# Optimization experiments

Measured on AMD Instinct MI355X. Metric: run time of the kernel, lower is better.

Reference implementation:

```python
import jax, jax.numpy as jnp
import numpy as np

B, T, D, H, DK, DV, FF = 4, 1024, 1024, 16, 64, 64, 4096


def setup_inputs() -> dict:
    key = jax.random.key(0)
    ks = jax.random.split(key, 16)
    sc = 0.02  # init scale (original uses uninitialized torch.empty; use small randn)
    n = lambda k, shape: jax.random.normal(k, shape, jnp.float32) * sc
    return dict(
        x=jax.random.normal(ks[0], (B, T, D), jnp.float32),
        y=jax.random.normal(ks[1], (B, T, D), jnp.float32),
        Wq1=n(ks[2], (H, D, DK)), Wk1=n(ks[3], (H, D, DK)),
        Wv1=n(ks[4], (H, D, DV)), Wo1=n(ks[5], (D, D)),
        Wq2=n(ks[6], (H, D, DK)), Wk2=n(ks[7], (H, D, DK)),
        Wv2=n(ks[8], (H, D, DV)), Wo2=n(ks[9], (D, D)),
        W_in=n(ks[10], (FF, D)), b_in=jnp.zeros((FF,), jnp.float32),
        W_out=n(ks[11], (D, FF)), b_out=jnp.zeros((D,), jnp.float32),
    )


def _mha(q, k, v, Wq, Wk, Wv, Wo):
    # per-head projections: (B,T,D) x (H,D,dk) -> (B,H,T,dk)
    WQ = jnp.einsum('btd,hdk->bhtk', q, Wq)
    WK = jnp.einsum('bsd,hdk->bhsk', k, Wk)
    WV = jnp.einsum('bsd,hdv->bhsv', v, Wv)
    scores = jnp.einsum('bhtk,bhsk->bhts', WQ, WK) / jnp.sqrt(jnp.float32(DK))
    # NOTE: original code softmaxes over dim=2 (the QUERY axis), kept faithfully
    attn = jax.nn.softmax(scores, axis=2)
    partial = jnp.einsum('bhts,bhsv->bhtv', attn, WV)
    partial = partial.transpose(0, 2, 1, 3).reshape(q.shape[0], q.shape[1], -1)  # (B,T,H*dv)
    return partial @ Wo


def _sub_norm(o):
    mean = o.mean(-1, keepdims=True)
    std = o.std(-1, ddof=1, keepdims=True)  # torch.std default is unbiased
    return o - mean - std  # faithful: subtract (not divide by) std


def reference(x, y, Wq1, Wk1, Wv1, Wo1, Wq2, Wk2, Wv2, Wo2, W_in, b_in, W_out, b_out):
    out1 = _sub_norm(_mha(y, y, y, Wq1, Wk1, Wv1, Wo1) + y)
    out2 = _sub_norm(_mha(y, x, x, Wq2, Wk2, Wv2, Wo2) + out1)
    ff = jax.nn.relu(y @ W_in.T + b_in) @ W_out.T + b_out  # FFN applied to y, as in source
    return _sub_norm(ff + out2)
```

## Files before the change

kernel.cpp:

```cpp
#include <hip/hip_runtime.h>


typedef unsigned short u16;
typedef __bf16 bf16x8 __attribute__((ext_vector_type(8)));
typedef float f32x4 __attribute__((ext_vector_type(4)));

__device__ __forceinline__ u16 f2bf(float f) {
    unsigned int u = __float_as_uint(f);
    u += 0x7fffu + ((u >> 16) & 1u);
    return (u16)(u >> 16);
}
__device__ __forceinline__ float bf2f(u16 b) {
    return __uint_as_float(((unsigned int)b) << 16);
}

typedef __attribute__((address_space(1))) const void* as1cv;
typedef __attribute__((address_space(3))) void* as3v;
__device__ __forceinline__ void gl_lds16(const void* g, void* l) {
    __builtin_amdgcn_global_load_lds((as1cv)g, (as3v)l, 16, 0, 0);
}


__global__ __launch_bounds__(256) void convert_f2b_k(const float* __restrict__ in, u16* __restrict__ out) {
    long i = (long)blockIdx.x * 256 + threadIdx.x;
    float4 v = reinterpret_cast<const float4*>(in)[i];
    ushort4 o;
    o.x = f2bf(v.x); o.y = f2bf(v.y); o.z = f2bf(v.z); o.w = f2bf(v.w);
    reinterpret_cast<ushort4*>(out)[i] = o;
}

__global__ __launch_bounds__(256) void pack_perm_t(const float* __restrict__ in, u16* __restrict__ out,
                                                   int Q, int R) {
    __shared__ float tile[64][65];
    int p = blockIdx.z;
    int r0 = blockIdx.x * 64, q0 = blockIdx.y * 64;
    int tx = threadIdx.x & 63, ty = threadIdx.x >> 6;
    const float* inp = in + ((long)p * Q + q0) * R + r0;
    #pragma unroll
    for (int i = 0; i < 64; i += 4)
        tile[ty + i][tx] = inp[(long)(ty + i) * R + tx];
    __syncthreads();
    u16* outp = out + ((long)p * R + r0) * Q + q0;
    #pragma unroll
    for (int i = 0; i < 64; i += 4)
        outp[(long)(ty + i) * Q + tx] = f2bf(tile[tx][ty + i]);
}

__global__ __launch_bounds__(256) void transpose_k(const u16* __restrict__ in, long ld_in, long z_in,
                                                   u16* __restrict__ out, long ld_out, long z_out) {
    __shared__ u16 tile[64][66];
    const u16* inz = in + (long)blockIdx.z * z_in;
    u16* outz = out + (long)blockIdx.z * z_out;
    int r0 = blockIdx.y * 64;
    int c0 = blockIdx.x * 64;
    int tx = threadIdx.x & 63, ty = threadIdx.x >> 6;
    #pragma unroll
    for (int i = 0; i < 64; i += 4)
        tile[ty + i][tx] = inz[(long)(r0 + ty + i) * ld_in + c0 + tx];
    __syncthreads();
    #pragma unroll
    for (int i = 0; i < 64; i += 4)
        outz[(long)(c0 + ty + i) * ld_out + r0 + tx] = tile[tx][ty + i];
}

template<int BM, int BN, int BK, int WM, int WN, int OUT_BF16, int EPI, int SWZ, int KS>
__global__ __launch_bounds__(256) void gemm_k(
    const u16* __restrict__ A, long lda, long a_zin, long a_zout,
    const u16* __restrict__ B, long ldb, long b_zin, long b_zout,
    void* __restrict__ Cv, long ldc, long c_zin, long c_zout,
    int zin, int K, float alpha, const float* __restrict__ bias,
    float* __restrict__ csum)
{
    static_assert(BK == 64, "staging assumes BK=64");
    constexpr int WTM = BM / WM;
    constexpr int WTN = BN / WN;
    constexpr int TM = WTM / 16;
    constexpr int TN = WTN / 16;
    __shared__ __align__(16) u16 smem[(BM + BN) * BK];
    u16* As = smem;
    u16* Bs = smem + BM * BK;

    int bx, by, z;
    if (SWZ == 4) {
        int L = blockIdx.x;
        if (KS > 1) { z = L >> 9; L &= 511; } else { z = 0; }
        by = (L & 7) * 4 + ((L >> 3) & 3);
        bx = L >> 5;
    } else {
        bx = blockIdx.x; by = blockIdx.y; z = blockIdx.z;
    }
    int zi = z % zin, zo = z / zin;
    A += (long)zi * a_zin + (long)zo * a_zout;
    B += (long)zi * b_zin + (long)zo * b_zout;
    long coff = (long)zi * c_zin + (long)zo * c_zout;

    int tid = threadIdx.x;
    int lane = tid & 63;
    int wave = tid >> 6;
    int wm = wave / WN, wn = wave % WN;
    long bm0 = (long)by * BM, bn0 = (long)bx * BN;

    f32x4 acc[TM][TN];
    #pragma unroll
    for (int i = 0; i < TM; ++i)
        #pragma unroll
        for (int j = 0; j < TN; ++j) {
            acc[i][j][0] = 0.f; acc[i][j][1] = 0.f;
            acc[i][j][2] = 0.f; acc[i][j][3] = 0.f;
        }

    int r16 = lane & 15;
    int quad = lane >> 4;
    int l8 = lane >> 3;
    int gsw = ((lane & 7) ^ l8) * 8;

    constexpr int ASTR = BM / 8;
    constexpr int BSTR = BN / 8;

    for (int k0 = 0; k0 < K; k0 += BK) {
        #pragma unroll
        for (int s = wave; s < ASTR; s += 4)
            gl_lds16(&A[(bm0 + s * 8 + l8) * lda + k0 + gsw], &As[s * 512]);
        #pragma unroll
        for (int s = wave; s < BSTR; s += 4)
            gl_lds16(&B[(bn0 + s * 8 + l8) * ldb + k0 + gsw], &Bs[s * 512]);
        __syncthreads();
        #pragma unroll
        for (int kk = 0; kk < BK; kk += 32) {
            int cb = (kk >> 3) + quad;
            bf16x8 av[TM], bv[TN];
            #pragma unroll
            for (int i = 0; i < TM; ++i) {
                int r = wm * WTM + i * 16 + r16;
                av[i] = *reinterpret_cast<const bf16x8*>(&As[r * 64 + ((cb ^ (r & 7)) * 8)]);
            }
            #pragma unroll
            for (int j = 0; j < TN; ++j) {
                int r = wn * WTN + j * 16 + r16;
                bv[j] = *reinterpret_cast<const bf16x8*>(&Bs[r * 64 + ((cb ^ (r & 7)) * 8)]);
            }
            #pragma unroll
            for (int i = 0; i < TM; ++i)
                #pragma unroll
                for (int j = 0; j < TN; ++j)
                    acc[i][j] = __builtin_amdgcn_mfma_f32_16x16x32_bf16(av[i], bv[j], acc[i][j], 0, 0, 0);
        }
        __syncthreads();
    }

    int rb = quad * 4;

    if (EPI == 4) {
        float csl[TN];
        #pragma unroll
        for (int j = 0; j < TN; ++j) csl[j] = 0.f;
        #pragma unroll
        for (int i = 0; i < TM; ++i)
            #pragma unroll
            for (int j = 0; j < TN; ++j)
                #pragma unroll
                for (int r = 0; r < 4; ++r)
                    csl[j] += __expf(acc[i][j][r] * alpha);
        #pragma unroll
        for (int j = 0; j < TN; ++j) {
            float cs = csl[j];
            cs += __shfl_xor(cs, 16, 64);
            cs += __shfl_xor(cs, 32, 64);
            if (quad == 0) {
                long col = bn0 + wn * WTN + j * 16 + r16;
                atomicAdd(&csum[((long)zo * zin + zi) * 1024 + col], cs);
            }
        }
        return;
    }

    constexpr int EB = OUT_BF16 ? 2 : 4;
    constexpr int CH = 16 / EB;
    constexpr int STRIDE = BN + CH;
    constexpr int LDSB = (BM + BN) * BK * 2;
    constexpr int EPASS = (BM * STRIDE * EB > LDSB) ? 2 : 1;
    constexpr int RPP = BM / EPASS;
    static_assert(RPP * STRIDE * EB <= LDSB, "epilogue tile overflows LDS");
    static_assert(EPASS == 1 || (WM == 2 && WTM == RPP), "pass/wave row alignment");
    constexpr int CPR = BN / CH;
    constexpr int NCH = RPP * CPR / 256;
    static_assert(RPP * CPR % 256 == 0, "store mapping");

    float* Ef = reinterpret_cast<float*>(smem);
    char* Cb = reinterpret_cast<char*>(Cv);

    for (int pass = 0; pass < EPASS; ++pass) {
        int p0 = pass * RPP;
        __syncthreads();
        #pragma unroll
        for (int i = 0; i < TM; ++i) {
            #pragma unroll
            for (int j = 0; j < TN; ++j) {
                int lcol = wn * WTN + j * 16 + r16;
                float bsv = (EPI == 1 || EPI == 2) ? bias[bn0 + lcol] : 0.f;
                #pragma unroll
                for (int r = 0; r < 4; ++r) {
                    int lrow = wm * WTM + i * 16 + rb + r;
                    if ((unsigned)(lrow - p0) < (unsigned)RPP) {
                        float v = acc[i][j][r] * alpha;
                        if (EPI == 1) { v += bsv; v = v > 0.f ? v : 0.f; }
                        else if (EPI == 2) { v += bsv; }
                        if (OUT_BF16) smem[(lrow - p0) * STRIDE + lcol] = f2bf(v);
                        else          Ef[(lrow - p0) * STRIDE + lcol] = v;
                    }
                }
            }
        }
        __syncthreads();
        #pragma unroll
        for (int c = 0; c < NCH; ++c) {
            int cid = tid + c * 256;
            int row = cid / CPR, ch = cid - row * CPR;
            int4 v = *reinterpret_cast<const int4*>(
                reinterpret_cast<const char*>(smem) + (row * STRIDE + ch * CH) * EB);
            long gidx = coff + (bm0 + p0 + row) * ldc + bn0 + ch * CH;
            *reinterpret_cast<int4*>(Cb + gidx * EB) = v;
        }
    }
}

__global__ __launch_bounds__(256) void attn_pv_k(
    const u16* __restrict__ Qg, long ldq, long qbz,
    const u16* __restrict__ Kg, long ldk, long kbz,
    const u16* __restrict__ Vg,
    u16* __restrict__ outg)
{
    __shared__ __align__(16) u16 Qs[128 * 64];
    __shared__ __align__(16) u16 Ks[64 * 64];
    __shared__ __align__(16) u16 Vs[64 * 64];
    __shared__ __align__(16) u16 Es[128 * 64];

    int L = blockIdx.x;
    int h  = (L & 7) * 2 + ((L >> 3) & 1);
    int tb = (L >> 4) & 7;
    int b  = L >> 7;

    const u16* Q  = Qg + (long)b * qbz + h * 64;
    const u16* Kp = Kg + (long)b * kbz + h * 64;
    const u16* Vp = Vg + (long)b * 1048576 + (long)h * 65536;
    u16* outp = outg + (long)b * 1048576 + (long)tb * 131072 + h * 64;

    int tid = threadIdx.x, lane = tid & 63, wave = tid >> 6;
    int wm = wave >> 1, wn = wave & 1;
    int r16 = lane & 15, quad = lane >> 4, l8 = lane >> 3;
    int gsw = ((lane & 7) ^ l8) * 8;
    long t0 = (long)tb * 128;

    #pragma unroll
    for (int s = wave; s < 16; s += 4)
        gl_lds16(&Q[(t0 + s * 8 + l8) * ldq + gsw], &Qs[s * 512]);

    f32x4 acc[4][2];
    #pragma unroll
    for (int i = 0; i < 4; ++i)
        #pragma unroll
        for (int j = 0; j < 2; ++j) {
            acc[i][j][0] = 0.f; acc[i][j][1] = 0.f;
            acc[i][j][2] = 0.f; acc[i][j][3] = 0.f;
        }

    for (int sc = 0; sc < 16; ++sc) {
        #pragma unroll
        for (int s = wave; s < 8; s += 4) {
            gl_lds16(&Kp[(long)(sc * 64 + s * 8 + l8) * ldk + gsw], &Ks[s * 512]);
            gl_lds16(&Vp[(long)(s * 8 + l8) * 1024 + sc * 64 + gsw], &Vs[s * 512]);
        }
        __syncthreads();

        f32x4 e[4][2];
        #pragma unroll
        for (int i = 0; i < 4; ++i)
            #pragma unroll
            for (int j = 0; j < 2; ++j) {
                e[i][j][0] = 0.f; e[i][j][1] = 0.f;
                e[i][j][2] = 0.f; e[i][j][3] = 0.f;
            }
        #pragma unroll
        for (int kk = 0; kk < 64; kk += 32) {
            int cb = (kk >> 3) + quad;
            bf16x8 av[4], bv[2];
            #pragma unroll
            for (int i = 0; i < 4; ++i) {
                int r = wm * 64 + i * 16 + r16;
                av[i] = *reinterpret_cast<const bf16x8*>(&Qs[r * 64 + ((cb ^ (r & 7)) * 8)]);
            }
            #pragma unroll
            for (int j = 0; j < 2; ++j) {
                int r = wn * 32 + j * 16 + r16;
                bv[j] = *reinterpret_cast<const bf16x8*>(&Ks[r * 64 + ((cb ^ (r & 7)) * 8)]);
            }
            #pragma unroll
            for (int i = 0; i < 4; ++i)
                #pragma unroll
                for (int j = 0; j < 2; ++j)
                    e[i][j] = __builtin_amdgcn_mfma_f32_16x16x32_bf16(av[i], bv[j], e[i][j], 0, 0, 0);
        }
        #pragma unroll
        for (int i = 0; i < 4; ++i)
            #pragma unroll
            for (int j = 0; j < 2; ++j) {
                int lcol = wn * 32 + j * 16 + r16;
                #pragma unroll
                for (int r = 0; r < 4; ++r) {
                    int lrow = wm * 64 + i * 16 + quad * 4 + r;
                    float v = __expf(e[i][j][r] * 0.125f);
                    Es[lrow * 64 + (((lcol >> 3) ^ (lrow & 7)) * 8) + (lcol & 7)] = f2bf(v);
                }
            }
        __syncthreads();

        #pragma unroll
        for (int kk = 0; kk < 64; kk += 32) {
            int cb = (kk >> 3) + quad;
            bf16x8 av[4], bv[2];
            #pragma unroll
            for (int i = 0; i < 4; ++i) {
                int r = wm * 64 + i * 16 + r16;
                av[i] = *reinterpret_cast<const bf16x8*>(&Es[r * 64 + ((cb ^ (r & 7)) * 8)]);
            }
            #pragma unroll
            for (int j = 0; j < 2; ++j) {
                int r = wn * 32 + j * 16 + r16;
                bv[j] = *reinterpret_cast<const bf16x8*>(&Vs[r * 64 + ((cb ^ (r & 7)) * 8)]);
            }
            #pragma unroll
            for (int i = 0; i < 4; ++i)
                #pragma unroll
                for (int j = 0; j < 2; ++j)
                    acc[i][j] = __builtin_amdgcn_mfma_f32_16x16x32_bf16(av[i], bv[j], acc[i][j], 0, 0, 0);
        }
        __syncthreads();
    }

    #pragma unroll
    for (int i = 0; i < 4; ++i)
        #pragma unroll
        for (int j = 0; j < 2; ++j) {
            int lcol = wn * 32 + j * 16 + r16;
            #pragma unroll
            for (int r = 0; r < 4; ++r) {
                int lrow = wm * 64 + i * 16 + quad * 4 + r;
                outp[(long)lrow * 1024 + lcol] = f2bf(acc[i][j][r]);
            }
        }
}

__global__ __launch_bounds__(256) void vscale_k(u16* __restrict__ Vt, const float* __restrict__ csum) {
    long idx = (long)blockIdx.x * 256 + threadIdx.x;
    int slab = (int)(idx >> 17);
    int rem = (int)(idx & 131071);
    int hv = rem >> 7;
    int s8 = (rem & 127) * 8;
    const float* cs = csum + slab * 16384 + (hv >> 6) * 1024 + s8;
    u16* pv = Vt + (long)slab * 1048576 + (long)hv * 1024 + s8;
    ushort4 a = *reinterpret_cast<ushort4*>(pv);
    ushort4 b = *reinterpret_cast<ushort4*>(pv + 4);
    a.x = f2bf(bf2f(a.x) / cs[0]); a.y = f2bf(bf2f(a.y) / cs[1]);
    a.z = f2bf(bf2f(a.z) / cs[2]); a.w = f2bf(bf2f(a.w) / cs[3]);
    b.x = f2bf(bf2f(b.x) / cs[4]); b.y = f2bf(bf2f(b.y) / cs[5]);
    b.z = f2bf(bf2f(b.z) / cs[6]); b.w = f2bf(bf2f(b.w) / cs[7]);
    *reinterpret_cast<ushort4*>(pv) = a;
    *reinterpret_cast<ushort4*>(pv + 4) = b;
}

template<int NP, int BIAS>
__global__ __launch_bounds__(256) void addsn_k(const float* __restrict__ parts, long pstride,
                                               const float* __restrict__ resid,
                                               const float* __restrict__ bias,
                                               float* __restrict__ out) {
    __shared__ float sm[8];
    long row = blockIdx.x;
    int tid = threadIdx.x;
    float4 x = reinterpret_cast<const float4*>(resid + row * 1024)[tid];
    #pragma unroll
    for (int p = 0; p < NP; ++p) {
        float4 a = reinterpret_cast<const float4*>(parts + p * pstride + row * 1024)[tid];
        x.x += a.x; x.y += a.y; x.z += a.z; x.w += a.w;
    }
    if (BIAS) {
        float4 bb = reinterpret_cast<const float4*>(bias)[tid];
        x.x += bb.x; x.y += bb.y; x.z += bb.z; x.w += bb.w;
    }
    float s = x.x + x.y + x.z + x.w;
    for (int o = 32; o > 0; o >>= 1) s += __shfl_down(s, o, 64);
    int lane = tid & 63, w = tid >> 6;
    if (lane == 0) sm[w] = s;
    __syncthreads();
    float mean = (sm[0] + sm[1] + sm[2] + sm[3]) * (1.f / 1024.f);
    float d0 = x.x - mean, d1 = x.y - mean, d2 = x.z - mean, d3 = x.w - mean;
    float q = d0 * d0 + d1 * d1 + d2 * d2 + d3 * d3;
    for (int o = 32; o > 0; o >>= 1) q += __shfl_down(q, o, 64);
    if (lane == 0) sm[w + 4] = q;
    __syncthreads();
    float sd = sqrtf((sm[4] + sm[5] + sm[6] + sm[7]) * (1.f / 1023.f));
    float4 ov;
    ov.x = d0 - sd; ov.y = d1 - sd; ov.z = d2 - sd; ov.w = d3 - sd;
    reinterpret_cast<float4*>(out + row * 1024)[tid] = ov;
}


extern "C" void kernel_launch(void* const* d_in, const int* in_sizes, int n_in,
                              void* d_out, int out_size, void* d_ws, size_t ws_size,
                              hipStream_t stream) {
    (void)in_sizes; (void)n_in; (void)out_size; (void)ws_size;
    const float* xf   = (const float*)d_in[0];
    const float* yf   = (const float*)d_in[1];
    const float* Wq1  = (const float*)d_in[2];
    const float* Wk1  = (const float*)d_in[3];
    const float* Wv1  = (const float*)d_in[4];
    const float* Wo1  = (const float*)d_in[5];
    const float* Wq2  = (const float*)d_in[6];
    const float* Wk2  = (const float*)d_in[7];
    const float* Wv2  = (const float*)d_in[8];
    const float* Wo2  = (const float*)d_in[9];
    const float* W_in = (const float*)d_in[10];
    const float* b_in = (const float*)d_in[11];
    const float* W_out= (const float*)d_in[12];
    const float* b_out= (const float*)d_in[13];

    char* p = (char*)d_ws;
    auto alloc = [&](size_t bytes) { char* r = p; p += bytes; return r; };
    u16*   yb    = (u16*)alloc(8388608);
    u16*   xb    = (u16*)alloc(8388608);
    u16*   W1cat = (u16*)alloc(8388608);
    u16*   Wkv2t = (u16*)alloc(4194304);
    u16*   Wo1t  = (u16*)alloc(2097152);
    u16*   Wo2t  = (u16*)alloc(2097152);
    u16*   Winb  = (u16*)alloc(8388608);
    u16*   Woutb = (u16*)alloc(8388608);
    u16*   QKV   = (u16*)alloc(33554432);
    u16*   KV2   = (u16*)alloc(16777216);
    u16*   Vt    = (u16*)alloc(8388608);
    u16*   Pb    = (u16*)alloc(33554432);
    float* csum  = (float*)alloc(262144);
    u16*   part  = (u16*)alloc(8388608);
    float* gout  = (float*)alloc(33554432);
    float* out1  = (float*)alloc(16777216);

    convert_f2b_k<<<4096, 256, 0, stream>>>(yf, yb);
    convert_f2b_k<<<4096, 256, 0, stream>>>(xf, xb);
    pack_perm_t<<<dim3(1, 16, 16), 256, 0, stream>>>(Wq1, W1cat,           1024, 64);
    pack_perm_t<<<dim3(1, 16, 16), 256, 0, stream>>>(Wk1, W1cat + 1048576, 1024, 64);
    pack_perm_t<<<dim3(1, 16, 16), 256, 0, stream>>>(Wv1, W1cat + 2097152, 1024, 64);
    pack_perm_t<<<dim3(1, 16, 16), 256, 0, stream>>>(Wq2, W1cat + 3145728, 1024, 64);
    pack_perm_t<<<dim3(1, 16, 16), 256, 0, stream>>>(Wk2, Wkv2t,           1024, 64);
    pack_perm_t<<<dim3(1, 16, 16), 256, 0, stream>>>(Wv2, Wkv2t + 1048576, 1024, 64);
    pack_perm_t<<<dim3(16, 16, 1), 256, 0, stream>>>(Wo1, Wo1t,            1024, 1024);
    pack_perm_t<<<dim3(16, 16, 1), 256, 0, stream>>>(Wo2, Wo2t,            1024, 1024);
    convert_f2b_k<<<4096, 256, 0, stream>>>(W_in,  Winb);
    convert_f2b_k<<<4096, 256, 0, stream>>>(W_out, Woutb);

    auto run_attention = [&](const u16* Q, long ldq, long qbz,
                             const u16* Kp, long ldk, long kbz,
                             const u16* Vp, long ldv, long vbz) {
        transpose_k<<<dim3(16, 16, 4), 256, 0, stream>>>(Vp, ldv, vbz, Vt, 1024L, 1048576L);
        hipMemsetAsync(csum, 0, 262144, stream);
        gemm_k<128,128,64,2,2,1,4,0,1><<<dim3(8, 8, 64), 256, 0, stream>>>(
            Q, ldq, 64L, qbz, Kp, ldk, 64L, kbz,
            (void*)Pb, 1024L, 0L, 0L, 16, 64, 0.125f, nullptr, csum);
        vscale_k<<<2048, 256, 0, stream>>>(Vt, csum);
        attn_pv_k<<<512, 256, 0, stream>>>(Q, ldq, qbz, Kp, ldk, kbz, Vt, part);
    };

    gemm_k<128,128,64,2,2,1,0,4,1><<<dim3(32 * 32), 256, 0, stream>>>(
        yb, 1024L, 0L, 0L, W1cat, 1024L, 0L, 0L, (void*)QKV, 4096L, 0L, 0L, 1, 1024, 1.0f, nullptr, nullptr);
    gemm_k<128,128,64,2,2,1,0,4,1><<<dim3(16 * 32), 256, 0, stream>>>(
        xb, 1024L, 0L, 0L, Wkv2t, 1024L, 0L, 0L, (void*)KV2, 2048L, 0L, 0L, 1, 1024, 1.0f, nullptr, nullptr);

    run_attention(QKV, 4096L, 4194304L, QKV + 1024, 4096L, 4194304L, QKV + 2048, 4096L, 4194304L);
    gemm_k<128,64,64,2,2,0,0,4,2><<<dim3(2 * 512), 256, 0, stream>>>(
        part, 1024L, 0L, 512L, Wo1t, 1024L, 0L, 512L,
        (void*)gout, 1024L, 0L, 4194304L, 1, 512, 1.0f, nullptr, nullptr);
    addsn_k<2,0><<<4096, 256, 0, stream>>>(gout, 4194304L, yf, nullptr, out1);

    run_attention(QKV + 3072, 4096L, 4194304L, KV2, 2048L, 2097152L, KV2 + 1024, 2048L, 2097152L);
    gemm_k<128,64,64,2,2,0,0,4,2><<<dim3(2 * 512), 256, 0, stream>>>(
        part, 1024L, 0L, 512L, Wo2t, 1024L, 0L, 512L,
        (void*)gout, 1024L, 0L, 4194304L, 1, 512, 1.0f, nullptr, nullptr);
    addsn_k<2,0><<<4096, 256, 0, stream>>>(gout, 4194304L, out1, nullptr, (float*)d_out);

    gemm_k<128,128,64,2,2,1,1,4,1><<<dim3(32 * 32), 256, 0, stream>>>(
        yb, 1024L, 0L, 0L, Winb, 1024L, 0L, 0L, (void*)Pb, 4096L, 0L, 0L, 1, 1024, 1.0f, b_in, nullptr);
    gemm_k<128,64,64,2,2,0,0,4,2><<<dim3(2 * 512), 256, 0, stream>>>(
        Pb, 4096L, 0L, 2048L, Woutb, 4096L, 0L, 2048L,
        (void*)gout, 1024L, 0L, 4194304L, 1, 2048, 1.0f, nullptr, nullptr);
    addsn_k<2,1><<<4096, 256, 0, stream>>>(gout, 4194304L, (const float*)d_out, b_out, (float*)d_out);
}
```

Baseline: 527.8 us.

## Add 256x256 eight-wave pipelined GEMM for projection and FFN matmuls

Introduces a new 512-thread GEMM kernel with 256x256 tiles and double-buffered LDS filled by direct global-to-LDS loads. Loads are staged in halves and interleaved with MFMA quarters under explicit vmcnt waits, barriers and setprio, so memory traffic overlaps compute. It replaces the QKV, KV2 and FFN-in GEMMs, and turns the FFN-out GEMM into a 4-way split-K whose extra partials go into the QKV buffer and are summed by addsn_k. The aim is higher MFMA utilisation and more tile reuse. In exchange there are fewer blocks, larger LDS use, and the QKV buffer is overwritten at the end.

```diff
diff --git a/kernel.cpp b/kernel.cpp
--- a/kernel.cpp
+++ b/kernel.cpp
@@ -224,6 +224,225 @@
     }
 }
 
+
+__device__ __forceinline__ void bar_raw() {
+    asm volatile("" ::: "memory");
+    __builtin_amdgcn_s_barrier();
+    asm volatile("" ::: "memory");
+}
+
+template<int N> __device__ __forceinline__ void vmw() {
+    if constexpr (N == 10) asm volatile("s_waitcnt vmcnt(10)" ::: "memory");
+    else if constexpr (N == 8) asm volatile("s_waitcnt vmcnt(8)" ::: "memory");
+    else if constexpr (N == 4) asm volatile("s_waitcnt vmcnt(4)" ::: "memory");
+    else if constexpr (N == 2) asm volatile("s_waitcnt vmcnt(2)" ::: "memory");
+    else if constexpr (N == 0) asm volatile("s_waitcnt vmcnt(0)" ::: "memory");
+}
+
+__device__ __forceinline__ void stage_half(const u16* __restrict__ base, long ld, int kt,
+                                           u16* __restrict__ lds, int half, int wave) {
+    const u16* src = base + (long)kt * 64;
+    #pragma unroll
+    for (int u = 0; u < 2; ++u) {
+        int s = half * 16 + u * 8 + wave;
+        gl_lds16(src + (long)(s * 8) * ld, lds + s * 512);
+    }
+}
+
+template<int IH>
+__device__ __forceinline__ void read_a8(bf16x8 (&av)[4][2], const u16* __restrict__ As,
+                                        int wm, int r16, int quad) {
+    #pragma unroll
+    for (int ii = 0; ii < 4; ++ii) {
+        int r = IH * 128 + wm * 64 + ii * 16 + r16;
+        #pragma unroll
+        for (int kx = 0; kx < 2; ++kx)
+            av[ii][kx] = *reinterpret_cast<const bf16x8*>(&As[r * 64 + (((kx * 4 + quad) ^ (r & 7)) * 8)]);
+    }
+}
+
+template<int JH>
+__device__ __forceinline__ void read_b8(bf16x8 (&bv)[2][2], const u16* __restrict__ Bs,
+                                        int wn, int r16, int quad) {
+    #pragma unroll
+    for (int j = 0; j < 2; ++j) {
+        int r = JH * 128 + wn * 32 + j * 16 + r16;
+        #pragma unroll
+        for (int kx = 0; kx < 2; ++kx)
+            bv[j][kx] = *reinterpret_cast<const bf16x8*>(&Bs[r * 64 + (((kx * 4 + quad) ^ (r & 7)) * 8)]);
+    }
+}
+
+template<int IH, int JH>
+__device__ __forceinline__ void mfma_q(f32x4 (&acc)[2][4][2][2],
+                                       const bf16x8 (&av)[4][2], const bf16x8 (&bv)[2][2]) {
+    #pragma unroll
+    for (int kx = 0; kx < 2; ++kx)
+        #pragma unroll
+        for (int ii = 0; ii < 4; ++ii)
+            #pragma unroll
+            for (int j = 0; j < 2; ++j)
+                acc[IH][ii][JH][j] = __builtin_amdgcn_mfma_f32_16x16x32_bf16(
+                    av[ii][kx], bv[j][kx], acc[IH][ii][JH][j], 0, 0, 0);
+}
+
+template<int MODE>
+__device__ __forceinline__ void tile_iter(
+    int t, f32x4 (&acc)[2][4][2][2], bf16x8 (&av)[4][2], bf16x8 (&bvh)[2][2][2],
+    u16* __restrict__ smem, const u16* __restrict__ Ab, long lda,
+    const u16* __restrict__ Bb, long ldb, int wave, int wm, int wn, int r16, int quad)
+{
+    u16* As0 = smem + (t & 1) * 32768;
+    u16* Bs0 = As0 + 16384;
+    u16* As1 = smem + ((t + 1) & 1) * 32768;
+    read_a8<0>(av, As0, wm, r16, quad);
+    read_b8<0>(bvh[0], Bs0, wn, r16, quad);
+    if (MODE < 2) stage_half(Ab, lda, t + 1, As1, 1, wave);
+    vmw<MODE == 0 ? 10 : (MODE == 1 ? 10 : 2)>();
+    bar_raw(); __builtin_amdgcn_sched_barrier(0);
+    __builtin_amdgcn_s_setprio(1);
+    mfma_q<0, 0>(acc, av, bvh[0]);
+    __builtin_amdgcn_s_setprio(0);
+    __builtin_amdgcn_sched_barrier(0);
+    bar_raw();
+    read_b8<1>(bvh[1], Bs0, wn, r16, quad);
+    if (MODE == 0) stage_half(Ab, lda, t + 2, As0, 0, wave);
+    vmw<MODE == 0 ? 10 : (MODE == 1 ? 8 : 0)>();
+    bar_raw(); __builtin_amdgcn_sched_barrier(0);
+    __builtin_amdgcn_s_setprio(1);
+    mfma_q<0, 1>(acc, av, bvh[1]);
+    __builtin_amdgcn_s_setprio(0);
+    __builtin_amdgcn_sched_barrier(0);
+    bar_raw();
+    read_a8<1>(av, As0, wm, r16, quad);
+    if (MODE == 0) stage_half(Bb, ldb, t + 2, Bs0, 0, wave);
+    bar_raw(); __builtin_amdgcn_sched_barrier(0);
+    __builtin_amdgcn_s_setprio(1);
+    mfma_q<1, 0>(acc, av, bvh[0]);
+    __builtin_amdgcn_s_setprio(0);
+    __builtin_amdgcn_sched_barrier(0);
+    bar_raw();
+    if (MODE == 0) stage_half(Bb, ldb, t + 2, Bs0, 1, wave);
+    if (MODE < 2) vmw<MODE == 0 ? 10 : 4>();
+    bar_raw(); __builtin_amdgcn_sched_barrier(0);
+    __builtin_amdgcn_s_setprio(1);
+    mfma_q<1, 1>(acc, av, bvh[1]);
+    __builtin_amdgcn_s_setprio(0);
+    __builtin_amdgcn_sched_barrier(0);
+    bar_raw();
+}
+
+template<int NT, int KS, int EPI, int OUT_BF16>
+__global__ __launch_bounds__(512, 2) void gemm8_k(
+    const u16* __restrict__ A, long lda,
+    const u16* __restrict__ B, long ldb,
+    void* __restrict__ Cv, void* __restrict__ Cv2, long ldc,
+    int K, float alpha, const float* __restrict__ bias, long czs)
+{
+    __shared__ __align__(16) u16 smem[65536];
+
+    int L = blockIdx.x;
+    int z = 0;
+    if (KS > 1) { z = L / (16 * NT); L -= z * 16 * NT; }
+    int by = (L & 7) * 2 + ((L >> 3) & 1);
+    int bx = L >> 4;
+    if (KS > 1) { A += (long)z * K; B += (long)z * K; }
+
+    int tid = threadIdx.x;
+    int lane = tid & 63, wave = tid >> 6;
+    int wm = wave >> 2, wn = wave & 3;
+    int r16 = lane & 15, quad = lane >> 4, l8 = lane >> 3;
+    int gsw = ((lane & 7) ^ l8) * 8;
+    long bm0 = (long)by * 256, bn0 = (long)bx * 256;
+    const u16* Ab = A + (bm0 + l8) * lda + gsw;
+    const u16* Bb = B + (bn0 + l8) * ldb + gsw;
+
+    f32x4 acc[2][4][2][2];
+    #pragma unroll
+    for (int a0 = 0; a0 < 2; ++a0)
+        #pragma unroll
+        for (int a1 = 0; a1 < 4; ++a1)
+            #pragma unroll
+            for (int a2 = 0; a2 < 2; ++a2)
+                #pragma unroll
+                for (int a3 = 0; a3 < 2; ++a3) {
+                    acc[a0][a1][a2][a3][0] = 0.f; acc[a0][a1][a2][a3][1] = 0.f;
+                    acc[a0][a1][a2][a3][2] = 0.f; acc[a0][a1][a2][a3][3] = 0.f;
+                }
+    bf16x8 av[4][2];
+    bf16x8 bvh[2][2][2];
+
+    int T = K >> 6;
+
+    stage_half(Ab, lda, 0, smem,         0, wave);
+    stage_half(Bb, ldb, 0, smem + 16384, 0, wave);
+    stage_half(Bb, ldb, 0, smem + 16384, 1, wave);
+    stage_half(Ab, lda, 0, smem,         1, wave);
+    stage_half(Ab, lda, 1, smem + 32768, 0, wave);
+    stage_half(Bb, ldb, 1, smem + 49152, 0, wave);
+    stage_half(Bb, ldb, 1, smem + 49152, 1, wave);
+    vmw<10>();
+    bar_raw();
+
+    for (int t = 0; t < T - 2; ++t)
+        tile_iter<0>(t, acc, av, bvh, smem, Ab, lda, Bb, ldb, wave, wm, wn, r16, quad);
+    tile_iter<1>(T - 2, acc, av, bvh, smem, Ab, lda, Bb, ldb, wave, wm, wn, r16, quad);
+    tile_iter<2>(T - 1, acc, av, bvh, smem, Ab, lda, Bb, ldb, wave, wm, wn, r16, quad);
+
+    constexpr int EB = OUT_BF16 ? 2 : 4;
+    constexpr int EPASS = OUT_BF16 ? 1 : 2;
+    char* Cb = reinterpret_cast<char*>((KS > 1 && z >= 2) ? Cv2 : Cv);
+    if (KS > 1) Cb += (long)(z & 1) * czs * EB;
+    float bsv[2][2];
+    if (EPI == 1) {
+        #pragma unroll
+        for (int jh = 0; jh < 2; ++jh)
+            #pragma unroll
+            for (int j = 0; j < 2; ++j)
+                bsv[jh][j] = bias[bn0 + jh * 128 + wn * 32 + j * 16 + r16];
+    }
+    u16* sm16 = smem;
+    float* smf = reinterpret_cast<float*>(smem);
+    #pragma unroll
+    for (int pass = 0; pass < EPASS; ++pass) {
+        bar_raw();
+        #pragma unroll
+        for (int ih = 0; ih < 2; ++ih) {
+            if (EPASS == 2 && ih != pass) continue;
+            #pragma unroll
+            for (int ii = 0; ii < 4; ++ii)
+                #pragma unroll
+                for (int jh = 0; jh < 2; ++jh)
+                    #pragma unroll
+                    for (int j = 0; j < 2; ++j)
+                        #pragma unroll
+                        for (int r = 0; r < 4; ++r) {
+                            int lrow = (EPASS == 2 ? 0 : ih * 128) + wm * 64 + ii * 16 + quad * 4 + r;
+                            int lcol = jh * 128 + wn * 32 + j * 16 + r16;
+                            float v = acc[ih][ii][jh][j][r] * alpha;
+                            if (EPI == 1) { v += bsv[jh][j]; v = v > 0.f ? v : 0.f; }
+                            int scol = lcol ^ ((lrow & 7) * 8);
+                            if (OUT_BF16) sm16[lrow * 256 + scol] = f2bf(v);
+                            else          smf[lrow * 256 + scol] = v;
+                        }
+        }
+        bar_raw();
+        constexpr int CH = 16 / EB;
+        constexpr int CPR = 256 / CH;
+        constexpr int NCH = (OUT_BF16 ? 256 : 128) * CPR / 512;
+        #pragma unroll
+        for (int c = 0; c < NCH; ++c) {
+            int cid = tid + c * 512;
+            int row = cid / CPR, ch = cid - row * CPR;
+            int col = (ch * CH) ^ ((row & 7) * 8);
+            int4 v = *reinterpret_cast<const int4*>(
+                reinterpret_cast<const char*>(smem) + ((long)row * 256 + col) * EB);
+            long grow = bm0 + pass * 128 + row;
+            *reinterpret_cast<int4*>(Cb + (grow * ldc + bn0 + ch * CH) * EB) = v;
+        }
+    }
+}
+
 __global__ __launch_bounds__(256) void attn_pv_k(
     const u16* __restrict__ Qg, long ldq, long qbz,
     const u16* __restrict__ Kg, long ldk, long kbz,
@@ -369,7 +588,9 @@
 }
 
 template<int NP, int BIAS>
-__global__ __launch_bounds__(256) void addsn_k(const float* __restrict__ parts, long pstride,
+__global__ __launch_bounds__(256) void addsn_k(const float* __restrict__ parts,
+                                               const float* __restrict__ parts2,
+                                               long pstride,
                                                const float* __restrict__ resid,
                                                const float* __restrict__ bias,
                                                float* __restrict__ out) {
@@ -379,7 +600,8 @@
     float4 x = reinterpret_cast<const float4*>(resid + row * 1024)[tid];
     #pragma unroll
     for (int p = 0; p < NP; ++p) {
-        float4 a = reinterpret_cast<const float4*>(parts + p * pstride + row * 1024)[tid];
+        const float* src = (p < 2) ? (parts + p * pstride) : (parts2 + (p - 2) * pstride);
+        float4 a = reinterpret_cast<const float4*>(src + row * 1024)[tid];
         x.x += a.x; x.y += a.y; x.z += a.z; x.w += a.w;
     }
     if (BIAS) {
@@ -467,27 +689,27 @@
         attn_pv_k<<<512, 256, 0, stream>>>(Q, ldq, qbz, Kp, ldk, kbz, Vt, part);
     };
 
-    gemm_k<128,128,64,2,2,1,0,4,1><<<dim3(32 * 32), 256, 0, stream>>>(
-        yb, 1024L, 0L, 0L, W1cat, 1024L, 0L, 0L, (void*)QKV, 4096L, 0L, 0L, 1, 1024, 1.0f, nullptr, nullptr);
-    gemm_k<128,128,64,2,2,1,0,4,1><<<dim3(16 * 32), 256, 0, stream>>>(
-        xb, 1024L, 0L, 0L, Wkv2t, 1024L, 0L, 0L, (void*)KV2, 2048L, 0L, 0L, 1, 1024, 1.0f, nullptr, nullptr);
+    gemm8_k<16,1,0,1><<<256, 512, 0, stream>>>(
+        yb, 1024L, W1cat, 1024L, (void*)QKV, nullptr, 4096L, 1024, 1.0f, nullptr, 0L);
+    gemm8_k<8,1,0,1><<<128, 512, 0, stream>>>(
+        xb, 1024L, Wkv2t, 1024L, (void*)KV2, nullptr, 2048L, 1024, 1.0f, nullptr, 0L);
 
     run_attention(QKV, 4096L, 4194304L, QKV + 1024, 4096L, 4194304L, QKV + 2048, 4096L, 4194304L);
     gemm_k<128,64,64,2,2,0,0,4,2><<<dim3(2 * 512), 256, 0, stream>>>(
         part, 1024L, 0L, 512L, Wo1t, 1024L, 0L, 512L,
         (void*)gout, 1024L, 0L, 4194304L, 1, 512, 1.0f, nullptr, nullptr);
-    addsn_k<2,0><<<4096, 256, 0, stream>>>(gout, 4194304L, yf, nullptr, out1);
+    addsn_k<2,0><<<4096, 256, 0, stream>>>(gout, nullptr, 4194304L, yf, nullptr, out1);
 
     run_attention(QKV + 3072, 4096L, 4194304L, KV2, 2048L, 2097152L, KV2 + 1024, 2048L, 2097152L);
     gemm_k<128,64,64,2,2,0,0,4,2><<<dim3(2 * 512), 256, 0, stream>>>(
         part, 1024L, 0L, 512L, Wo2t, 1024L, 0L, 512L,
         (void*)gout, 1024L, 0L, 4194304L, 1, 512, 1.0f, nullptr, nullptr);
-    addsn_k<2,0><<<4096, 256, 0, stream>>>(gout, 4194304L, out1, nullptr, (float*)d_out);
-
-    gemm_k<128,128,64,2,2,1,1,4,1><<<dim3(32 * 32), 256, 0, stream>>>(
-        yb, 1024L, 0L, 0L, Winb, 1024L, 0L, 0L, (void*)Pb, 4096L, 0L, 0L, 1, 1024, 1.0f, b_in, nullptr);
-    gemm_k<128,64,64,2,2,0,0,4,2><<<dim3(2 * 512), 256, 0, stream>>>(
-        Pb, 4096L, 0L, 2048L, Woutb, 4096L, 0L, 2048L,
-        (void*)gout, 1024L, 0L, 4194304L, 1, 2048, 1.0f, nullptr, nullptr);
-    addsn_k<2,1><<<4096, 256, 0, stream>>>(gout, 4194304L, (const float*)d_out, b_out, (float*)d_out);
-}
+    addsn_k<2,0><<<4096, 256, 0, stream>>>(gout, nullptr, 4194304L, out1, nullptr, (float*)d_out);
+
+    gemm8_k<16,1,1,1><<<256, 512, 0, stream>>>(
+        yb, 1024L, Winb, 1024L, (void*)Pb, nullptr, 4096L, 1024, 1.0f, b_in, 0L);
+    gemm8_k<4,4,0,0><<<256, 512, 0, stream>>>(
+        Pb, 4096L, Woutb, 4096L, (void*)gout, (void*)QKV, 1024L, 1024, 1.0f, nullptr, 4194304L);
+    addsn_k<4,1><<<4096, 256, 0, stream>>>(gout, (const float*)QKV, 4194304L,
+                                           (const float*)d_out, b_out, (float*)d_out);
+}
```

Measured after the change: 518.3 us. No clear change (-1.8%).
